# Kernel tuning notes

Hardware: AMD Instinct MI355X
Metric: run time of the kernel (lower is better)

The kernel has to match this reference:

```python
import jax, jax.numpy as jnp
import numpy as np

EPS_D = 1e-05
EPS_LOG = 1e-05
H_BAND = 0.5


def setup_inputs() -> dict:
    key = jax.random.key(0)
    k1, k2 = jax.random.split(key)
    N, C, Hh, Ww = 4, 256, 64, 64
    y = jax.random.normal(k1, (N, C, Hh, Ww), dtype=jnp.float32)
    y_hat = jax.random.normal(k2, (N, C, Hh, Ww), dtype=jnp.float32)
    return {"y": y, "y_hat": y_hat}


def contextual_loss(x, y, h=H_BAND):
    # x, y: (N, C, H, W)
    N, C, Hh, Ww = x.shape
    # mean over W, H, N of y -> per-channel mu, broadcast as (1, C, 1, 1)
    y_mu = y.mean(axis=3).mean(axis=2).mean(axis=0).reshape(1, C, 1, 1)
    x_c = x - y_mu
    y_c = y - y_mu
    x_n = x_c / jnp.linalg.norm(x_c, ord=2, axis=1, keepdims=True)
    y_n = y_c / jnp.linalg.norm(y_c, ord=2, axis=1, keepdims=True)
    x_n = x_n.reshape(N, C, Hh * Ww)  # (N, C, P)
    y_n = y_n.reshape(N, C, Hh * Ww)
    # cosine similarity: (N, P, P)
    cosine_sim = jnp.einsum('ncp,ncq->npq', x_n, y_n)
    d = 1.0 - cosine_sim
    d_min = jnp.min(d, axis=2, keepdims=True)
    d_tilde = d / (d_min + EPS_D)
    w = jnp.exp((1.0 - d_tilde) / h)
    cx_ij = w / jnp.sum(w, axis=2, keepdims=True)
    cx = jnp.mean(jnp.max(cx_ij, axis=1), axis=1)  # (N,)
    return jnp.mean(-jnp.log(cx + EPS_LOG))


def reference(y, y_hat):
    return contextual_loss(y, y_hat)
```

## Files before the change

kernel.cpp:

```cpp
#include <hip/hip_runtime.h>
#include <hip/hip_bf16.h>
#include <math.h>


namespace {
constexpr int NB = 4;
constexpr int C  = 256;
constexpr int P  = 4096;
constexpr float EPSD = 1e-5f;
constexpr float EPSL = 1e-5f;
constexpr float HB   = 0.5f;

constexpr size_t OFF_MU    = 0;
constexpr size_t OFF_XNT   = 256;
constexpr size_t OFF_YNT   = OFF_XNT + (size_t)NB * P * C / 2;
constexpr size_t OFF_RMAX  = OFF_YNT + (size_t)NB * P * C / 2;
constexpr size_t OFF_ALPHA = OFF_RMAX + (size_t)NB * P;
constexpr size_t OFF_LROW  = OFF_ALPHA + (size_t)NB * P;
constexpr size_t OFF_CPART = OFF_LROW + (size_t)NB * P;
}

typedef __attribute__((ext_vector_type(8))) __bf16 bf16x8;
typedef __attribute__((ext_vector_type(16))) float f32x16;
typedef unsigned short u16;

__device__ __forceinline__ bf16x8 ldfrag(const u16* p) {
  return *reinterpret_cast<const bf16x8*>(p);
}
__device__ __forceinline__ void gload_lds16(const u16* g, u16* l) {
  __builtin_amdgcn_global_load_lds(
      (const __attribute__((address_space(1))) void*)g,
      (__attribute__((address_space(3))) void*)l, 16, 0, 0);
}
__device__ __forceinline__ f32x16 zero16() {
  f32x16 z;
#pragma unroll
  for (int i = 0; i < 16; ++i) z[i] = 0.f;
  return z;
}

__device__ __forceinline__ void stage_tile(const u16* __restrict__ src, int row0,
                                           u16* lds, int t) {
#pragma unroll
  for (int i = 0; i < 8; ++i) {
    const int g  = i * 512 + t;
    const int r  = g >> 5;
    const int gs = (g & 31) ^ (r & 15);
    gload_lds16(src + (size_t)(row0 + r) * 256 + gs * 8, lds + (size_t)g * 8);
  }
}

__global__ void k_mu(const float* __restrict__ yh, float* __restrict__ ws) {
  const int c = blockIdx.x;
  const int t = threadIdx.x;
  float s = 0.f;
  for (int n = 0; n < NB; ++n) {
    const float* base = yh + ((size_t)(n * C + c)) * P;
    for (int p = t; p < P; p += 256) s += base[p];
  }
  __shared__ float red[256];
  red[t] = s;
  __syncthreads();
  for (int w = 128; w > 0; w >>= 1) {
    if (t < w) red[t] += red[t + w];
    __syncthreads();
  }
  if (t == 0) ws[OFF_MU + c] = red[0] * (1.0f / (NB * P));
}

__global__ __launch_bounds__(256) void k_norm(const float* __restrict__ x,
                                              const float* __restrict__ yh,
                                              float* __restrict__ ws) {
  const int b     = blockIdx.x;
  const int arr   = b & 1;
  const int strip = (b >> 1) & 63;
  const int n     = b >> 7;
  const int t     = threadIdx.x;
  const int w     = t >> 6;
  const int l     = t & 63;

  __shared__ float mu_s[C];
  __shared__ float tile[64][257];
  __shared__ float red[4][64];
  __shared__ float invs[64];

  mu_s[t] = ws[OFF_MU + t];
  __syncthreads();

  const float* src = arr ? yh : x;
  const size_t base = ((size_t)n * C) * P + (size_t)strip * 64 + l;
  float ssq = 0.f;
  for (int cc = 0; cc < C; cc += 4) {
    const int c = cc + w;
    const float v = src[base + (size_t)c * P] - mu_s[c];
    tile[l][c] = v;
    ssq += v * v;
  }
  red[w][l] = ssq;
  __syncthreads();
  if (t < 64) invs[t] = 1.0f / sqrtf(red[0][t] + red[1][t] + red[2][t] + red[3][t]);
  __syncthreads();

  uint* dst = reinterpret_cast<uint*>(ws + (arr ? OFF_YNT : OFF_XNT));
  const int c2 = t & 127;
  const size_t drow = ((size_t)n * P + (size_t)strip * 64) * (C / 2);
  for (int it = 0; it < 32; ++it) {
    const int pl = it * 2 + (t >> 7);
    const float s  = invs[pl];
    const float v0 = tile[pl][2 * c2] * s;
    const float v1 = tile[pl][2 * c2 + 1] * s;
    const unsigned short u0 = __builtin_bit_cast(unsigned short, __float2bfloat16(v0));
    const unsigned short u1 = __builtin_bit_cast(unsigned short, __float2bfloat16(v1));
    dst[drow + (size_t)pl * (C / 2) + c2] = ((uint)u1 << 16) | u0;
  }
}

template <int PASS>
__global__ __launch_bounds__(512, 2) void k_row(float* __restrict__ ws) {
  const int t = threadIdx.x;
  const int wave = t >> 6, l = t & 63, l31 = l & 31, lh = l >> 5;
  const int rt = wave >> 2, ct = wave & 3;
  const int n  = blockIdx.x >> 6;
  const int p0 = (blockIdx.x & 63) << 6;

  const u16* xn = reinterpret_cast<const u16*>(ws + OFF_XNT) + (size_t)n * P * C;
  const u16* yn = reinterpret_cast<const u16*>(ws + OFF_YNT) + (size_t)n * P * C;

  __shared__ __align__(16) u16 Bl[2][128 * 256];
  __shared__ float red[8][32];

  const u16* Ap = xn + (size_t)(p0 + rt * 32 + l31) * 256;
  bf16x8 af[16];
#pragma unroll
  for (int ks = 0; ks < 16; ++ks) af[ks] = ldfrag(Ap + (ks * 2 + lh) * 8);

  float av[16], rm[16];
  if (PASS == 1) {
#pragma unroll
    for (int r = 0; r < 16; ++r) {
      const int row = (r & 3) + 8 * (r >> 2) + 4 * lh;
      const int p = p0 + rt * 32 + row;
      av[r] = ws[OFF_ALPHA + (size_t)n * P + p];
      rm[r] = ws[OFF_RMAX + (size_t)n * P + p];
    }
  }

  float run[16];
#pragma unroll
  for (int r = 0; r < 16; ++r) run[r] = (PASS == 0) ? -3.0e38f : 0.f;

  stage_tile(yn, 0, Bl[0], t);
  __syncthreads();

  const int q_local = ct * 32 + l31;
  const int qsw = q_local & 15;
  const u16* Brow0 = &Bl[0][(size_t)q_local * 256];
  const u16* Brow1 = &Bl[1][(size_t)q_local * 256];

  for (int step = 0; step < 32; ++step) {
    const int cur = step & 1;
    if (step + 1 < 32) stage_tile(yn, (step + 1) * 128, Bl[cur ^ 1], t);
    const u16* Brow = cur ? Brow1 : Brow0;

    f32x16 acc0 = zero16(), acc1 = zero16();
#pragma unroll
    for (int ks = 0; ks < 16; ks += 2) {
      acc0 = __builtin_amdgcn_mfma_f32_32x32x16_bf16(
          af[ks], ldfrag(Brow + (((ks * 2 + lh)) ^ qsw) * 8), acc0, 0, 0, 0);
      acc1 = __builtin_amdgcn_mfma_f32_32x32x16_bf16(
          af[ks + 1], ldfrag(Brow + (((ks * 2 + 2 + lh)) ^ qsw) * 8), acc1, 0, 0, 0);
    }
    const f32x16 acc = acc0 + acc1;

    if (PASS == 0) {
#pragma unroll
      for (int r = 0; r < 16; ++r) run[r] = fmaxf(run[r], acc[r]);
    } else {
#pragma unroll
      for (int r = 0; r < 16; ++r) run[r] += __expf(av[r] * (acc[r] - rm[r]));
    }
    __syncthreads();
  }

#pragma unroll
  for (int m = 1; m <= 16; m <<= 1) {
#pragma unroll
    for (int r = 0; r < 16; ++r) {
      const float o = __shfl_xor(run[r], m, 64);
      run[r] = (PASS == 0) ? fmaxf(run[r], o) : (run[r] + o);
    }
  }
  if (l31 == 0) {
#pragma unroll
    for (int r = 0; r < 16; ++r)
      red[wave][(r & 3) + 8 * (r >> 2) + 4 * lh] = run[r];
  }
  __syncthreads();
  if (t < 64) {
    const int rt2 = t >> 5, row = t & 31;
    const int p = p0 + rt2 * 32 + row;
    if (PASS == 0) {
      float v = red[rt2 * 4][row];
#pragma unroll
      for (int j = 1; j < 4; ++j) v = fmaxf(v, red[rt2 * 4 + j][row]);
      ws[OFF_RMAX + (size_t)n * P + p]  = v;
      ws[OFF_ALPHA + (size_t)n * P + p] = 1.0f / (HB * (1.0f - v + EPSD));
    } else {
      float s = red[rt2 * 4][row];
#pragma unroll
      for (int j = 1; j < 4; ++j) s += red[rt2 * 4 + j][row];
      const float a_ = ws[OFF_ALPHA + (size_t)n * P + p];
      const float m_ = ws[OFF_RMAX + (size_t)n * P + p];
      ws[OFF_LROW + (size_t)n * P + p] = a_ * m_ + logf(s);
    }
  }
}

__global__ __launch_bounds__(512, 2) void k_col(float* __restrict__ ws) {
  const int t = threadIdx.x;
  const int wave = t >> 6, l = t & 63, l31 = l & 31, lh = l >> 5;
  const int rt = wave >> 2, ct = wave & 3;
  const int n  = blockIdx.x >> 6;
  const int q0 = (blockIdx.x & 63) << 6;

  const u16* xn = reinterpret_cast<const u16*>(ws + OFF_XNT) + (size_t)n * P * C;
  const u16* yn = reinterpret_cast<const u16*>(ws + OFF_YNT) + (size_t)n * P * C;
  const float* alp = ws + OFF_ALPHA + (size_t)n * P;
  const float* lrw = ws + OFF_LROW + (size_t)n * P;

  __shared__ __align__(16) u16 Bl[2][128 * 256];
  __shared__ float red[8][32];

  const u16* Ap = yn + (size_t)(q0 + rt * 32 + l31) * 256;
  bf16x8 af[16];
#pragma unroll
  for (int ks = 0; ks < 16; ++ks) af[ks] = ldfrag(Ap + (ks * 2 + lh) * 8);

  float run[16];
#pragma unroll
  for (int r = 0; r < 16; ++r) run[r] = -3.0e38f;

  stage_tile(xn, 0, Bl[0], t);
  __syncthreads();

  const int p_local = ct * 32 + l31;
  const int psw = p_local & 15;
  const u16* Brow0 = &Bl[0][(size_t)p_local * 256];
  const u16* Brow1 = &Bl[1][(size_t)p_local * 256];

  for (int step = 0; step < 32; ++step) {
    const int cur = step & 1;
    if (step + 1 < 32) stage_tile(xn, (step + 1) * 128, Bl[cur ^ 1], t);
    const u16* Brow = cur ? Brow1 : Brow0;

    const int pcol = step * 128 + p_local;
    const float a_ = alp[pcol];
    const float L_ = lrw[pcol];

    f32x16 acc0 = zero16(), acc1 = zero16();
#pragma unroll
    for (int ks = 0; ks < 16; ks += 2) {
      acc0 = __builtin_amdgcn_mfma_f32_32x32x16_bf16(
          af[ks], ldfrag(Brow + (((ks * 2 + lh)) ^ psw) * 8), acc0, 0, 0, 0);
      acc1 = __builtin_amdgcn_mfma_f32_32x32x16_bf16(
          af[ks + 1], ldfrag(Brow + (((ks * 2 + 2 + lh)) ^ psw) * 8), acc1, 0, 0, 0);
    }
    const f32x16 acc = acc0 + acc1;
#pragma unroll
    for (int r = 0; r < 16; ++r) run[r] = fmaxf(run[r], fmaf(a_, acc[r], -L_));
    __syncthreads();
  }

#pragma unroll
  for (int m = 1; m <= 16; m <<= 1) {
#pragma unroll
    for (int r = 0; r < 16; ++r) run[r] = fmaxf(run[r], __shfl_xor(run[r], m, 64));
  }
  if (l31 == 0) {
#pragma unroll
    for (int r = 0; r < 16; ++r)
      red[wave][(r & 3) + 8 * (r >> 2) + 4 * lh] = run[r];
  }
  __syncthreads();
  if (t < 64) {
    const int rt2 = t >> 5, row = t & 31;
    float v = red[rt2 * 4][row];
#pragma unroll
    for (int j = 1; j < 4; ++j) v = fmaxf(v, red[rt2 * 4 + j][row]);
    float e = __expf(v);
#pragma unroll
    for (int m = 1; m <= 32; m <<= 1) e += __shfl_xor(e, m, 64);
    if (t == 0) ws[OFF_CPART + (size_t)n * 64 + (q0 >> 6)] = e;
  }
}

__global__ void k_final(const float* __restrict__ ws, float* __restrict__ out) {
  const int t = threadIdx.x;
  __shared__ float per_n[NB];
  if (t < NB) {
    float s = 0.f;
    for (int i = 0; i < 64; ++i) s += ws[OFF_CPART + (size_t)t * 64 + i];
    per_n[t] = -logf(s * (1.0f / P) + EPSL);
  }
  __syncthreads();
  if (t == 0)
    out[0] = 0.25f * (per_n[0] + per_n[1] + per_n[2] + per_n[3]);
}

extern "C" void kernel_launch(void* const* d_in, const int* in_sizes, int n_in,
                              void* d_out, int out_size, void* d_ws, size_t ws_size,
                              hipStream_t stream) {
  const float* x  = (const float*)d_in[0];
  const float* yh = (const float*)d_in[1];
  float* ws  = (float*)d_ws;
  float* out = (float*)d_out;

  k_mu<<<dim3(C), dim3(256), 0, stream>>>(yh, ws);
  k_norm<<<dim3(NB * 64 * 2), dim3(256), 0, stream>>>(x, yh, ws);
  k_row<0><<<dim3(NB * 64), dim3(512), 0, stream>>>(ws);
  k_row<1><<<dim3(NB * 64), dim3(512), 0, stream>>>(ws);
  k_col<<<dim3(NB * 64), dim3(512), 0, stream>>>(ws);
  k_final<<<dim3(1), dim3(64), 0, stream>>>(ws, out);
}
```

Baseline: 189.8 us.

## Retile row/col kernels to 128x128 tiles with split-Q halves and merge kernels

Each block now covers 128 rows and half of the other dimension (2048 columns), and each wave computes a 32x64 tile with four accumulators, so every A fragment in registers is used twice per LDS B read. Partial row max, row sum and column max are written per half and combined by new small k_alpha and k_L kernels, and by a reworked k_final. This roughly halves B-tile staging per output element and improves MFMA density. The cost is two extra kernel launches and extra accumulator registers.

```diff
diff --git a/kernel.cpp b/kernel.cpp
--- a/kernel.cpp
+++ b/kernel.cpp
@@ -14,10 +14,12 @@
 constexpr size_t OFF_MU    = 0;
 constexpr size_t OFF_XNT   = 256;
 constexpr size_t OFF_YNT   = OFF_XNT + (size_t)NB * P * C / 2;
-constexpr size_t OFF_RMAX  = OFF_YNT + (size_t)NB * P * C / 2;
+constexpr size_t OFF_RMAXH = OFF_YNT + (size_t)NB * P * C / 2;
+constexpr size_t OFF_SUMH  = OFF_RMAXH + (size_t)NB * 2 * P;
+constexpr size_t OFF_CMAXH = OFF_SUMH + (size_t)NB * 2 * P;
+constexpr size_t OFF_RMAX  = OFF_CMAXH + (size_t)NB * 2 * P;
 constexpr size_t OFF_ALPHA = OFF_RMAX + (size_t)NB * P;
 constexpr size_t OFF_LROW  = OFF_ALPHA + (size_t)NB * P;
-constexpr size_t OFF_CPART = OFF_LROW + (size_t)NB * P;
 }
 
 typedef __attribute__((ext_vector_type(8))) __bf16 bf16x8;
@@ -118,10 +120,12 @@
 template <int PASS>
 __global__ __launch_bounds__(512, 2) void k_row(float* __restrict__ ws) {
   const int t = threadIdx.x;
-  const int wave = t >> 6, l = t & 63, l31 = l & 31, lh = l >> 5;
-  const int rt = wave >> 2, ct = wave & 3;
-  const int n  = blockIdx.x >> 6;
-  const int p0 = (blockIdx.x & 63) << 6;
+  const int wave = t >> 6, l = t & 63, l31 = l & 31, lh = l >> 5, l15 = l31 & 15;
+  const int rt = wave >> 1, ct = wave & 1;
+  const int bid = blockIdx.x;
+  const int qhalf = bid & 1, n = (bid >> 1) & 3, strip = bid >> 3;
+  const int p0 = strip * 128;
+  const int qbase = qhalf * 2048;
 
   const u16* xn = reinterpret_cast<const u16*>(ws + OFF_XNT) + (size_t)n * P * C;
   const u16* yn = reinterpret_cast<const u16*>(ws + OFF_YNT) + (size_t)n * P * C;
@@ -134,14 +138,15 @@
 #pragma unroll
   for (int ks = 0; ks < 16; ++ks) af[ks] = ldfrag(Ap + (ks * 2 + lh) * 8);
 
-  float av[16], rm[16];
+  float av[16], arm[16];
   if (PASS == 1) {
 #pragma unroll
     for (int r = 0; r < 16; ++r) {
       const int row = (r & 3) + 8 * (r >> 2) + 4 * lh;
       const int p = p0 + rt * 32 + row;
-      av[r] = ws[OFF_ALPHA + (size_t)n * P + p];
-      rm[r] = ws[OFF_RMAX + (size_t)n * P + p];
+      const float a_ = ws[OFF_ALPHA + (size_t)n * P + p];
+      av[r]  = a_;
+      arm[r] = a_ * ws[OFF_RMAX + (size_t)n * P + p];
     }
   }
 
@@ -149,35 +154,36 @@
 #pragma unroll
   for (int r = 0; r < 16; ++r) run[r] = (PASS == 0) ? -3.0e38f : 0.f;
 
-  stage_tile(yn, 0, Bl[0], t);
-  __syncthreads();
-
-  const int q_local = ct * 32 + l31;
-  const int qsw = q_local & 15;
-  const u16* Brow0 = &Bl[0][(size_t)q_local * 256];
-  const u16* Brow1 = &Bl[1][(size_t)q_local * 256];
-
-  for (int step = 0; step < 32; ++step) {
+  stage_tile(yn, qbase, Bl[0], t);
+  __syncthreads();
+
+  const int r0 = ct * 64 + l31;
+
+  for (int step = 0; step < 16; ++step) {
     const int cur = step & 1;
-    if (step + 1 < 32) stage_tile(yn, (step + 1) * 128, Bl[cur ^ 1], t);
-    const u16* Brow = cur ? Brow1 : Brow0;
-
-    f32x16 acc0 = zero16(), acc1 = zero16();
+    if (step + 1 < 16) stage_tile(yn, qbase + (step + 1) * 128, Bl[cur ^ 1], t);
+    const u16* Brow = &Bl[cur][(size_t)r0 * 256];
+
+    f32x16 a00 = zero16(), a01 = zero16(), a10 = zero16(), a11 = zero16();
 #pragma unroll
     for (int ks = 0; ks < 16; ks += 2) {
-      acc0 = __builtin_amdgcn_mfma_f32_32x32x16_bf16(
-          af[ks], ldfrag(Brow + (((ks * 2 + lh)) ^ qsw) * 8), acc0, 0, 0, 0);
-      acc1 = __builtin_amdgcn_mfma_f32_32x32x16_bf16(
-          af[ks + 1], ldfrag(Brow + (((ks * 2 + 2 + lh)) ^ qsw) * 8), acc1, 0, 0, 0);
-    }
-    const f32x16 acc = acc0 + acc1;
+      const int g0 = ((ks * 2 + lh) ^ l15) * 8;
+      const int g1 = ((ks * 2 + 2 + lh) ^ l15) * 8;
+      a00 = __builtin_amdgcn_mfma_f32_32x32x16_bf16(af[ks], ldfrag(Brow + g0), a00, 0, 0, 0);
+      a10 = __builtin_amdgcn_mfma_f32_32x32x16_bf16(af[ks], ldfrag(Brow + 32 * 256 + g0), a10, 0, 0, 0);
+      a01 = __builtin_amdgcn_mfma_f32_32x32x16_bf16(af[ks + 1], ldfrag(Brow + g1), a01, 0, 0, 0);
+      a11 = __builtin_amdgcn_mfma_f32_32x32x16_bf16(af[ks + 1], ldfrag(Brow + 32 * 256 + g1), a11, 0, 0, 0);
+    }
+    const f32x16 s0 = a00 + a01;
+    const f32x16 s1 = a10 + a11;
 
     if (PASS == 0) {
 #pragma unroll
-      for (int r = 0; r < 16; ++r) run[r] = fmaxf(run[r], acc[r]);
+      for (int r = 0; r < 16; ++r) run[r] = fmaxf(run[r], fmaxf(s0[r], s1[r]));
     } else {
 #pragma unroll
-      for (int r = 0; r < 16; ++r) run[r] += __expf(av[r] * (acc[r] - rm[r]));
+      for (int r = 0; r < 16; ++r)
+        run[r] += __expf(fmaf(av[r], s0[r], -arm[r])) + __expf(fmaf(av[r], s1[r], -arm[r]));
     }
     __syncthreads();
   }
@@ -196,32 +202,44 @@
       red[wave][(r & 3) + 8 * (r >> 2) + 4 * lh] = run[r];
   }
   __syncthreads();
-  if (t < 64) {
+  if (t < 128) {
     const int rt2 = t >> 5, row = t & 31;
-    const int p = p0 + rt2 * 32 + row;
-    if (PASS == 0) {
-      float v = red[rt2 * 4][row];
-#pragma unroll
-      for (int j = 1; j < 4; ++j) v = fmaxf(v, red[rt2 * 4 + j][row]);
-      ws[OFF_RMAX + (size_t)n * P + p]  = v;
-      ws[OFF_ALPHA + (size_t)n * P + p] = 1.0f / (HB * (1.0f - v + EPSD));
-    } else {
-      float s = red[rt2 * 4][row];
-#pragma unroll
-      for (int j = 1; j < 4; ++j) s += red[rt2 * 4 + j][row];
-      const float a_ = ws[OFF_ALPHA + (size_t)n * P + p];
-      const float m_ = ws[OFF_RMAX + (size_t)n * P + p];
-      ws[OFF_LROW + (size_t)n * P + p] = a_ * m_ + logf(s);
-    }
-  }
+    const float v0 = red[rt2 * 2][row], v1 = red[rt2 * 2 + 1][row];
+    const size_t o = (size_t)(n * 2 + qhalf) * P + p0 + rt2 * 32 + row;
+    if (PASS == 0)
+      ws[OFF_RMAXH + o] = fmaxf(v0, v1);
+    else
+      ws[OFF_SUMH + o] = v0 + v1;
+  }
+}
+
+__global__ void k_alpha(float* __restrict__ ws) {
+  const int i = blockIdx.x * 256 + threadIdx.x;
+  const int n = i >> 12, p = i & (P - 1);
+  const float rm = fmaxf(ws[OFF_RMAXH + (size_t)(n * 2) * P + p],
+                         ws[OFF_RMAXH + (size_t)(n * 2 + 1) * P + p]);
+  ws[OFF_RMAX + (size_t)n * P + p]  = rm;
+  ws[OFF_ALPHA + (size_t)n * P + p] = 1.0f / (HB * (1.0f - rm + EPSD));
+}
+
+__global__ void k_L(float* __restrict__ ws) {
+  const int i = blockIdx.x * 256 + threadIdx.x;
+  const int n = i >> 12, p = i & (P - 1);
+  const float s = ws[OFF_SUMH + (size_t)(n * 2) * P + p] +
+                  ws[OFF_SUMH + (size_t)(n * 2 + 1) * P + p];
+  const float a_ = ws[OFF_ALPHA + (size_t)n * P + p];
+  const float rm = ws[OFF_RMAX + (size_t)n * P + p];
+  ws[OFF_LROW + (size_t)n * P + p] = fmaf(a_, rm, logf(s));
 }
 
 __global__ __launch_bounds__(512, 2) void k_col(float* __restrict__ ws) {
   const int t = threadIdx.x;
-  const int wave = t >> 6, l = t & 63, l31 = l & 31, lh = l >> 5;
-  const int rt = wave >> 2, ct = wave & 3;
-  const int n  = blockIdx.x >> 6;
-  const int q0 = (blockIdx.x & 63) << 6;
+  const int wave = t >> 6, l = t & 63, l31 = l & 31, lh = l >> 5, l15 = l31 & 15;
+  const int rt = wave >> 1, ct = wave & 1;
+  const int bid = blockIdx.x;
+  const int phalf = bid & 1, n = (bid >> 1) & 3, qstrip = bid >> 3;
+  const int q0 = qstrip * 128;
+  const int pbase = phalf * 2048;
 
   const u16* xn = reinterpret_cast<const u16*>(ws + OFF_XNT) + (size_t)n * P * C;
   const u16* yn = reinterpret_cast<const u16*>(ws + OFF_YNT) + (size_t)n * P * C;
@@ -240,34 +258,35 @@
 #pragma unroll
   for (int r = 0; r < 16; ++r) run[r] = -3.0e38f;
 
-  stage_tile(xn, 0, Bl[0], t);
-  __syncthreads();
-
-  const int p_local = ct * 32 + l31;
-  const int psw = p_local & 15;
-  const u16* Brow0 = &Bl[0][(size_t)p_local * 256];
-  const u16* Brow1 = &Bl[1][(size_t)p_local * 256];
-
-  for (int step = 0; step < 32; ++step) {
+  stage_tile(xn, pbase, Bl[0], t);
+  __syncthreads();
+
+  const int r0 = ct * 64 + l31;
+
+  for (int step = 0; step < 16; ++step) {
     const int cur = step & 1;
-    if (step + 1 < 32) stage_tile(xn, (step + 1) * 128, Bl[cur ^ 1], t);
-    const u16* Brow = cur ? Brow1 : Brow0;
-
-    const int pcol = step * 128 + p_local;
-    const float a_ = alp[pcol];
-    const float L_ = lrw[pcol];
-
-    f32x16 acc0 = zero16(), acc1 = zero16();
+    if (step + 1 < 16) stage_tile(xn, pbase + (step + 1) * 128, Bl[cur ^ 1], t);
+    const u16* Brow = &Bl[cur][(size_t)r0 * 256];
+
+    const int pc0 = pbase + step * 128 + ct * 64 + l31;
+    const float a0 = alp[pc0],      L0 = lrw[pc0];
+    const float a1 = alp[pc0 + 32], L1 = lrw[pc0 + 32];
+
+    f32x16 a00 = zero16(), a01 = zero16(), a10 = zero16(), a11 = zero16();
 #pragma unroll
     for (int ks = 0; ks < 16; ks += 2) {
-      acc0 = __builtin_amdgcn_mfma_f32_32x32x16_bf16(
-          af[ks], ldfrag(Brow + (((ks * 2 + lh)) ^ psw) * 8), acc0, 0, 0, 0);
-      acc1 = __builtin_amdgcn_mfma_f32_32x32x16_bf16(
-          af[ks + 1], ldfrag(Brow + (((ks * 2 + 2 + lh)) ^ psw) * 8), acc1, 0, 0, 0);
-    }
-    const f32x16 acc = acc0 + acc1;
-#pragma unroll
-    for (int r = 0; r < 16; ++r) run[r] = fmaxf(run[r], fmaf(a_, acc[r], -L_));
+      const int g0 = ((ks * 2 + lh) ^ l15) * 8;
+      const int g1 = ((ks * 2 + 2 + lh) ^ l15) * 8;
+      a00 = __builtin_amdgcn_mfma_f32_32x32x16_bf16(af[ks], ldfrag(Brow + g0), a00, 0, 0, 0);
+      a10 = __builtin_amdgcn_mfma_f32_32x32x16_bf16(af[ks], ldfrag(Brow + 32 * 256 + g0), a10, 0, 0, 0);
+      a01 = __builtin_amdgcn_mfma_f32_32x32x16_bf16(af[ks + 1], ldfrag(Brow + g1), a01, 0, 0, 0);
+      a11 = __builtin_amdgcn_mfma_f32_32x32x16_bf16(af[ks + 1], ldfrag(Brow + 32 * 256 + g1), a11, 0, 0, 0);
+    }
+    const f32x16 s0 = a00 + a01;
+    const f32x16 s1 = a10 + a11;
+#pragma unroll
+    for (int r = 0; r < 16; ++r)
+      run[r] = fmaxf(run[r], fmaxf(fmaf(a0, s0[r], -L0), fmaf(a1, s1[r], -L1)));
     __syncthreads();
   }
 
@@ -282,29 +301,36 @@
       red[wave][(r & 3) + 8 * (r >> 2) + 4 * lh] = run[r];
   }
   __syncthreads();
-  if (t < 64) {
+  if (t < 128) {
     const int rt2 = t >> 5, row = t & 31;
-    float v = red[rt2 * 4][row];
-#pragma unroll
-    for (int j = 1; j < 4; ++j) v = fmaxf(v, red[rt2 * 4 + j][row]);
-    float e = __expf(v);
-#pragma unroll
-    for (int m = 1; m <= 32; m <<= 1) e += __shfl_xor(e, m, 64);
-    if (t == 0) ws[OFF_CPART + (size_t)n * 64 + (q0 >> 6)] = e;
+    const float v = fmaxf(red[rt2 * 2][row], red[rt2 * 2 + 1][row]);
+    ws[OFF_CMAXH + (size_t)(n * 2 + phalf) * P + q0 + rt2 * 32 + row] = v;
   }
 }
 
 __global__ void k_final(const float* __restrict__ ws, float* __restrict__ out) {
   const int t = threadIdx.x;
-  __shared__ float per_n[NB];
-  if (t < NB) {
-    float s = 0.f;
-    for (int i = 0; i < 64; ++i) s += ws[OFF_CPART + (size_t)t * 64 + i];
-    per_n[t] = -logf(s * (1.0f / P) + EPSL);
-  }
-  __syncthreads();
-  if (t == 0)
-    out[0] = 0.25f * (per_n[0] + per_n[1] + per_n[2] + per_n[3]);
+  __shared__ float red[256];
+  __shared__ float lsum_s;
+  if (t == 0) lsum_s = 0.f;
+  for (int n = 0; n < NB; ++n) {
+    float e = 0.f;
+    for (int q = t; q < P; q += 256) {
+      const float m = fmaxf(ws[OFF_CMAXH + (size_t)(n * 2) * P + q],
+                            ws[OFF_CMAXH + (size_t)(n * 2 + 1) * P + q]);
+      e += __expf(m);
+    }
+    __syncthreads();
+    red[t] = e;
+    __syncthreads();
+    for (int w = 128; w > 0; w >>= 1) {
+      if (t < w) red[t] += red[t + w];
+      __syncthreads();
+    }
+    if (t == 0) lsum_s += -logf(red[0] * (1.0f / P) + EPSL);
+  }
+  __syncthreads();
+  if (t == 0) out[0] = lsum_s * 0.25f;
 }
 
 extern "C" void kernel_launch(void* const* d_in, const int* in_sizes, int n_in,
@@ -317,8 +343,10 @@
 
   k_mu<<<dim3(C), dim3(256), 0, stream>>>(yh, ws);
   k_norm<<<dim3(NB * 64 * 2), dim3(256), 0, stream>>>(x, yh, ws);
-  k_row<0><<<dim3(NB * 64), dim3(512), 0, stream>>>(ws);
-  k_row<1><<<dim3(NB * 64), dim3(512), 0, stream>>>(ws);
-  k_col<<<dim3(NB * 64), dim3(512), 0, stream>>>(ws);
-  k_final<<<dim3(1), dim3(64), 0, stream>>>(ws, out);
-}
+  k_row<0><<<dim3(256), dim3(512), 0, stream>>>(ws);
+  k_alpha<<<dim3(NB * P / 256), dim3(256), 0, stream>>>(ws);
+  k_row<1><<<dim3(256), dim3(512), 0, stream>>>(ws);
+  k_L<<<dim3(NB * P / 256), dim3(256), 0, stream>>>(ws);
+  k_col<<<dim3(256), dim3(512), 0, stream>>>(ws);
+  k_final<<<dim3(1), dim3(256), 0, stream>>>(ws, out);
+}
```

After: 173.5 us. -8.6%, faster.
